# Optimization experiments

Hardware: AMD Instinct MI355X
Metric: run time of the kernel (lower is better)

Reference implementation:

```python
import jax, jax.numpy as jnp
import numpy as np

N = 131072
IN_C1 = 64
MED_C = 64
OUT_C = 64
EPS = 1e-8


def _glorot(key, shape):
    fan_in = shape[0]
    bound = 1.0 / np.sqrt(fan_in)
    return jax.random.uniform(key, shape, jnp.float32, -bound, bound)


def setup_inputs() -> dict:
    key = jax.random.key(0)
    ks = jax.random.split(key, 16)
    inp = {
        "key_value_input": jax.random.normal(ks[0], (N, IN_C1), jnp.float32),
        "query_input": jax.random.normal(ks[1], (N, 7), jnp.float32),
        # Linear params stored as [in, out] (y = x @ W + b)
        "key_W": _glorot(ks[2], (IN_C1, MED_C)), "key_b": jnp.zeros((MED_C,), jnp.float32),
        "value_W": _glorot(ks[3], (IN_C1, MED_C)), "value_b": jnp.zeros((MED_C,), jnp.float32),
        "T_W": _glorot(ks[4], (7, MED_C * MED_C)), "T_b": jnp.zeros((MED_C * MED_C,), jnp.float32),
        "d1_W": _glorot(ks[5], (MED_C, 64)), "d1_b": jnp.zeros((64,), jnp.float32),
        "d2_W": _glorot(ks[6], (64, 32)), "d2_b": jnp.zeros((32,), jnp.float32),
        "d3_W": _glorot(ks[7], (32, OUT_C)), "d3_b": jnp.zeros((OUT_C,), jnp.float32),
        "scale": jnp.float32(1.0),
    }
    return inp


def reference(key_value_input, query_input, key_W, key_b, value_W, value_b,
              T_W, T_b, d1_W, d1_b, d2_W, d2_b, d3_W, d3_b, scale):
    # Per-token hypernetwork: T [N, med_c, med_c]
    T = (query_input @ T_W + T_b).reshape(-1, MED_C, MED_C)
    k = key_value_input @ key_W + key_b              # [N, med_c]
    v = key_value_input @ value_W + value_b          # [N, med_c]
    # query = T @ kv  (batched mat-vec)
    q = jnp.einsum('nij,nj->ni', T, key_value_input)  # [N, med_c]
    att = q * k
    # F.normalize(p=2, dim=-1, eps=1e-8): x / max(||x||_2, eps)
    norm = jnp.linalg.norm(att, axis=-1, keepdims=True)
    att = att / jnp.maximum(norm, EPS)
    v = jax.nn.softmax(v * scale, axis=-1)
    x = att * v
    # small MLP head d
    h = jax.nn.relu(x @ d1_W + d1_b)
    h = jax.nn.relu(h @ d2_W + d2_b)
    return h @ d3_W + d3_b
```

## Files before the change

### kernel.cpp

```cpp
#include <hip/hip_runtime.h>
#include <math.h>

typedef _Float16 f16_t;
typedef __attribute__((ext_vector_type(8))) _Float16 f16x8;
typedef __attribute__((ext_vector_type(4))) float f32x4;

#define NTOK 131072
#define MT   128
#define TPB  256
#define RP16 72
#define OP32 68
#define SLABB 4608

#define OFF_KEY 0
#define OFF_VAL 4096
#define OFF_T   8192
#define OFF_D1  40960
#define OFF_D2  45056
#define OFF_D3  47104
#define WTOT    49152

__device__ __forceinline__ f32x4 mfma1(f16x8 a, f16x8 b, f32x4 c) {
    return __builtin_amdgcn_mfma_f32_16x16x32_f16(a, b, c, 0, 0, 0);
}

struct B2 { f16x8 b0, b1; };

__device__ __forceinline__ B2 loadB_lds(const f16_t* __restrict__ b, int c, int l15, int quad) {
    const char* base = (const char*)b;
    int o0 = (16 * c + l15) * 128 + quad * 16;
    int sw = (l15 & 7) << 4;
    B2 r;
    r.b0 = *(const f16x8*)(base + (o0 ^ sw));
    r.b1 = *(const f16x8*)(base + ((o0 + 64) ^ sw));
    return r;
}

#define GEMML(buf, c, a00, a01, a10, a11, acc0, acc1) do {        \
    B2 Bf = loadB_lds((buf), (c), l15, quad);                      \
    acc0 = mfma1(a01, Bf.b1, mfma1(a00, Bf.b0, acc0));             \
    acc1 = mfma1(a11, Bf.b1, mfma1(a10, Bf.b0, acc1));             \
} while (0)

__device__ __forceinline__ void gl_lds16(const void* g, void* l) {
    __builtin_amdgcn_global_load_lds(
        (const __attribute__((address_space(1))) unsigned int*)g,
        (__attribute__((address_space(3))) unsigned int*)l, 16, 0, 0);
}

__device__ __forceinline__ void stage8k(const f16_t* __restrict__ gsrc, f16_t* lbuf, int tid) {
#pragma unroll
    for (int i = 0; i < 2; ++i) {
        int o = (i * 256 + tid) * 16;
        int g = o ^ (((o >> 7) & 7) << 4);
        gl_lds16((const char*)gsrc + g, (char*)lbuf + (o & ~1023));
    }
}
__device__ __forceinline__ void stage4k_r128(const f16_t* __restrict__ gsrc, f16_t* lbuf, int tid) {
    int o = tid * 16;
    int g = o ^ (((o >> 7) & 7) << 4);
    gl_lds16((const char*)gsrc + g, (char*)lbuf + (o & ~1023));
}
__device__ __forceinline__ void stage4k_r64(const f16_t* __restrict__ gsrc, f16_t* lbuf, int tid) {
    int o = tid * 16;
    int g = o ^ (((o >> 7) & 3) << 4);
    gl_lds16((const char*)gsrc + g, (char*)lbuf + (o & ~1023));
}

#define VMW2() asm volatile("s_waitcnt vmcnt(2)" ::: "memory")
#define VMW0() asm volatile("s_waitcnt vmcnt(0)" ::: "memory")
#define BAR()  do { __builtin_amdgcn_s_barrier(); asm volatile("" ::: "memory"); } while (0)

__global__ __launch_bounds__(256)
void prep_w(const float* __restrict__ keyW, const float* __restrict__ valW,
            const float* __restrict__ TW,   const float* __restrict__ TB,
            const float* __restrict__ d1W,  const float* __restrict__ d2W,
            const float* __restrict__ d3W,  f16_t* __restrict__ wsf)
{
    int idx = blockIdx.x * 256 + threadIdx.x;
    if (idx >= WTOT) return;
    float src;
    if (idx < OFF_VAL) {
        int r = idx - OFF_KEY, n = r >> 6, j = r & 63;
        src = keyW[j * 64 + n];
    } else if (idx < OFF_T) {
        int r = idx - OFF_VAL, n = r >> 6, j = r & 63;
        src = valW[j * 64 + n];
    } else if (idx < OFF_D1) {
        int r = idx - OFF_T, p = r >> 12, q = r & 4095;
        src = (p < 7) ? TW[p * 4096 + q] : TB[q];
    } else if (idx < OFF_D2) {
        int r = idx - OFF_D1, n = r >> 6, j = r & 63;
        src = d1W[j * 64 + n];
    } else if (idx < OFF_D3) {
        int r = idx - OFF_D2, n = r >> 6, j = r & 63;
        src = d2W[j * 32 + n];
    } else {
        int r = idx - OFF_D3, n = r >> 5, j = r & 31;
        src = d3W[j * 64 + n];
    }
    wsf[idx] = (f16_t)src;
}

__device__ __forceinline__ void front_rt(
    f16_t* __restrict__ Rf,
    const f16_t* __restrict__ keyb, const f16_t* __restrict__ valb,
    int l15, int quad, int rtb,
    f16x8 a0, f16x8 a1,
    f32x4 q0, f32x4 q1, f32x4 q2, f32x4 q3,
    f32x4 kbv, f32x4 vbv, float sc)
{
    f32x4 k0 = {}, k1 = {}, k2 = {}, k3 = {}, v0 = {}, v1 = {}, v2 = {}, v3 = {};
    { B2 B = loadB_lds(keyb, 0, l15, quad); k0 = mfma1(a1, B.b1, mfma1(a0, B.b0, k0)); }
    { B2 B = loadB_lds(keyb, 1, l15, quad); k1 = mfma1(a1, B.b1, mfma1(a0, B.b0, k1)); }
    { B2 B = loadB_lds(keyb, 2, l15, quad); k2 = mfma1(a1, B.b1, mfma1(a0, B.b0, k2)); }
    { B2 B = loadB_lds(keyb, 3, l15, quad); k3 = mfma1(a1, B.b1, mfma1(a0, B.b0, k3)); }
    { B2 B = loadB_lds(valb, 0, l15, quad); v0 = mfma1(a1, B.b1, mfma1(a0, B.b0, v0)); }
    { B2 B = loadB_lds(valb, 1, l15, quad); v1 = mfma1(a1, B.b1, mfma1(a0, B.b0, v1)); }
    { B2 B = loadB_lds(valb, 2, l15, quad); v2 = mfma1(a1, B.b1, mfma1(a0, B.b0, v2)); }
    { B2 B = loadB_lds(valb, 3, l15, quad); v3 = mfma1(a1, B.b1, mfma1(a0, B.b0, v3)); }

    f32x4 sv0 = (v0 + vbv[0]) * sc;
    f32x4 sv1 = (v1 + vbv[1]) * sc;
    f32x4 sv2 = (v2 + vbv[2]) * sc;
    f32x4 sv3 = (v3 + vbv[3]) * sc;

    f32x4 mx;
#pragma unroll
    for (int e = 0; e < 4; ++e)
        mx[e] = fmaxf(fmaxf(sv0[e], sv1[e]), fmaxf(sv2[e], sv3[e]));
#pragma unroll
    for (int m = 1; m < 16; m <<= 1)
#pragma unroll
        for (int e = 0; e < 4; ++e) mx[e] = fmaxf(mx[e], __shfl_xor(mx[e], m, 64));
#pragma unroll
    for (int e = 0; e < 4; ++e) {
        sv0[e] = __expf(sv0[e] - mx[e]);
        sv1[e] = __expf(sv1[e] - mx[e]);
        sv2[e] = __expf(sv2[e] - mx[e]);
        sv3[e] = __expf(sv3[e] - mx[e]);
    }
    f32x4 se = sv0 + sv1 + sv2 + sv3;
#pragma unroll
    for (int m = 1; m < 16; m <<= 1)
#pragma unroll
        for (int e = 0; e < 4; ++e) se[e] += __shfl_xor(se[e], m, 64);

    f32x4 at0 = q0 * (k0 + kbv[0]);
    f32x4 at1 = q1 * (k1 + kbv[1]);
    f32x4 at2 = q2 * (k2 + kbv[2]);
    f32x4 at3 = q3 * (k3 + kbv[3]);
    f32x4 nr = at0 * at0 + at1 * at1 + at2 * at2 + at3 * at3;
#pragma unroll
    for (int m = 1; m < 16; m <<= 1)
#pragma unroll
        for (int e = 0; e < 4; ++e) nr[e] += __shfl_xor(nr[e], m, 64);

    f32x4 fac;
#pragma unroll
    for (int e = 0; e < 4; ++e)
        fac[e] = 1.0f / (fmaxf(sqrtf(nr[e]), 1e-8f) * se[e]);

#pragma unroll
    for (int e = 0; e < 4; ++e) {
        f16_t* rr = Rf + (rtb + quad * 4 + e) * RP16 + l15;
        rr[0]  = (f16_t)(at0[e] * sv0[e] * fac[e]);
        rr[16] = (f16_t)(at1[e] * sv1[e] * fac[e]);
        rr[32] = (f16_t)(at2[e] * sv2[e] * fac[e]);
        rr[48] = (f16_t)(at3[e] * sv3[e] * fac[e]);
    }
}

__global__ __launch_bounds__(TPB, 2)
void fused_mfma(const float* __restrict__ kv_in, const float* __restrict__ q_in,
                const float* __restrict__ keyB,  const float* __restrict__ valB,
                const float* __restrict__ d1B,   const float* __restrict__ d2B,
                const float* __restrict__ d3B,   const float* __restrict__ scale_p,
                const f16_t* __restrict__ wsf,   float* __restrict__ out)
{
    __shared__ __align__(16) unsigned char Slab[4][SLABB];
    __shared__ __align__(16) float Qs[8][MT];
    __shared__ __align__(16) f16_t WB[2][4096];

    const int tid  = threadIdx.x;
    const int wv   = tid >> 6, lane = tid & 63;
    const int quad = lane >> 4, l15 = lane & 15;
    const int RB   = wv * 32;
    const long t0  = (long)blockIdx.x * MT;

    f16_t* __restrict__ Rf = (f16_t*)Slab[wv];
    float* __restrict__ Of = (float*)Slab[wv];

    stage8k(wsf + OFF_T + 0 * 4096, WB[0], tid);
    stage8k(wsf + OFF_T + 1 * 4096, WB[1], tid);

    {
        const int r = lane >> 1, half = lane & 1;
        const float4* p4 = (const float4*)(kv_in + (t0 + RB + r) * 64 + half * 32);
        f16_t* dst = Rf + r * RP16 + half * 32;
#pragma unroll
        for (int b = 0; b < 4; ++b) {
            float4 f0 = p4[2 * b], f1 = p4[2 * b + 1];
            f16x8 h;
            h[0] = (f16_t)f0.x; h[1] = (f16_t)f0.y; h[2] = (f16_t)f0.z; h[3] = (f16_t)f0.w;
            h[4] = (f16_t)f1.x; h[5] = (f16_t)f1.y; h[6] = (f16_t)f1.z; h[7] = (f16_t)f1.w;
            *(f16x8*)(dst + 8 * b) = h;
        }
    }
    if (lane < 32) {
        const float* qp = q_in + (t0 + RB + lane) * 7;
#pragma unroll
        for (int p = 0; p < 7; ++p) Qs[p][RB + lane] = qp[p];
        Qs[7][RB + lane] = 1.0f;
    }

    f32x4 kbv, vbv;
#pragma unroll
    for (int c = 0; c < 4; ++c) { kbv[c] = keyB[16 * c + l15]; vbv[c] = valB[16 * c + l15]; }
    const float sc = scale_p[0];

    f16x8 ah00 = *(const f16x8*)(Rf + l15 * RP16 + quad * 8);
    f16x8 ah01 = *(const f16x8*)(Rf + l15 * RP16 + 32 + quad * 8);
    f16x8 ah10 = *(const f16x8*)(Rf + (16 + l15) * RP16 + quad * 8);
    f16x8 ah11 = *(const f16x8*)(Rf + (16 + l15) * RP16 + 32 + quad * 8);

    f32x4 q00 = {}, q01 = {}, q02 = {}, q03 = {};
    f32x4 q10 = {}, q11 = {}, q12 = {}, q13 = {};
#pragma unroll 1
    for (int p = 0; p < 8; ++p) {
        const f16_t* tb = WB[p & 1];
        VMW2(); BAR();
        f32x4 t00 = {}, t01 = {}, t02 = {}, t03 = {};
        f32x4 t10 = {}, t11 = {}, t12 = {}, t13 = {};
        GEMML(tb, 0, ah00, ah01, ah10, ah11, t00, t10);
        GEMML(tb, 1, ah00, ah01, ah10, ah11, t01, t11);
        GEMML(tb, 2, ah00, ah01, ah10, ah11, t02, t12);
        GEMML(tb, 3, ah00, ah01, ah10, ah11, t03, t13);
        f32x4 qp0 = *(const f32x4*)&Qs[p][RB + quad * 4];
        f32x4 qp1 = *(const f32x4*)&Qs[p][RB + 16 + quad * 4];
        q00 += qp0 * t00; q01 += qp0 * t01; q02 += qp0 * t02; q03 += qp0 * t03;
        q10 += qp1 * t10; q11 += qp1 * t11; q12 += qp1 * t12; q13 += qp1 * t13;
        BAR();
        const f16_t* nsrc = (p < 6) ? (wsf + OFF_T + (p + 2) * 4096)
                                    : ((p == 6) ? (wsf + OFF_KEY) : (wsf + OFF_VAL));
        stage8k(nsrc, WB[p & 1], tid);
    }
    VMW0(); BAR();

    front_rt(Rf, WB[0], WB[1], l15, quad, 0,  ah00, ah01, q00, q01, q02, q03, kbv, vbv, sc);
    front_rt(Rf, WB[0], WB[1], l15, quad, 16, ah10, ah11, q10, q11, q12, q13, kbv, vbv, sc);
    BAR();
    stage8k(wsf + OFF_D1, WB[0], tid);
    stage4k_r128(wsf + OFF_D2, WB[1], tid);
    stage4k_r64 (wsf + OFF_D3, WB[1] + 2048, tid);
    VMW0(); BAR();

    f16x8 xh00 = *(const f16x8*)(Rf + l15 * RP16 + quad * 8);
    f16x8 xh01 = *(const f16x8*)(Rf + l15 * RP16 + 32 + quad * 8);
    f16x8 xh10 = *(const f16x8*)(Rf + (16 + l15) * RP16 + quad * 8);
    f16x8 xh11 = *(const f16x8*)(Rf + (16 + l15) * RP16 + 32 + quad * 8);
    {
        f32x4 h00 = {}, h01 = {}, h02 = {}, h03 = {};
        f32x4 h10 = {}, h11 = {}, h12 = {}, h13 = {};
        GEMML(WB[0], 0, xh00, xh01, xh10, xh11, h00, h10);
        GEMML(WB[0], 1, xh00, xh01, xh10, xh11, h01, h11);
        GEMML(WB[0], 2, xh00, xh01, xh10, xh11, h02, h12);
        GEMML(WB[0], 3, xh00, xh01, xh10, xh11, h03, h13);
        f32x4 b1v;
#pragma unroll
        for (int c = 0; c < 4; ++c) b1v[c] = d1B[16 * c + l15];
#pragma unroll
        for (int e = 0; e < 4; ++e) {
            f16_t* r0 = Rf + (quad * 4 + e) * RP16 + l15;
            r0[0]  = (f16_t)fmaxf(h00[e] + b1v[0], 0.f);
            r0[16] = (f16_t)fmaxf(h01[e] + b1v[1], 0.f);
            r0[32] = (f16_t)fmaxf(h02[e] + b1v[2], 0.f);
            r0[48] = (f16_t)fmaxf(h03[e] + b1v[3], 0.f);
            f16_t* r1 = Rf + (16 + quad * 4 + e) * RP16 + l15;
            r1[0]  = (f16_t)fmaxf(h10[e] + b1v[0], 0.f);
            r1[16] = (f16_t)fmaxf(h11[e] + b1v[1], 0.f);
            r1[32] = (f16_t)fmaxf(h12[e] + b1v[2], 0.f);
            r1[48] = (f16_t)fmaxf(h13[e] + b1v[3], 0.f);
        }
    }

    xh00 = *(const f16x8*)(Rf + l15 * RP16 + quad * 8);
    xh01 = *(const f16x8*)(Rf + l15 * RP16 + 32 + quad * 8);
    xh10 = *(const f16x8*)(Rf + (16 + l15) * RP16 + quad * 8);
    xh11 = *(const f16x8*)(Rf + (16 + l15) * RP16 + 32 + quad * 8);
    {
        f32x4 g00 = {}, g01 = {}, g10 = {}, g11 = {};
        GEMML(WB[1], 0, xh00, xh01, xh10, xh11, g00, g10);
        GEMML(WB[1], 1, xh00, xh01, xh10, xh11, g01, g11);
        float b20 = d2B[l15], b21 = d2B[16 + l15];
#pragma unroll
        for (int e = 0; e < 4; ++e) {
            f16_t* r0 = Rf + (quad * 4 + e) * RP16 + l15;
            r0[0]  = (f16_t)fmaxf(g00[e] + b20, 0.f);
            r0[16] = (f16_t)fmaxf(g01[e] + b21, 0.f);
            f16_t* r1 = Rf + (16 + quad * 4 + e) * RP16 + l15;
            r1[0]  = (f16_t)fmaxf(g10[e] + b20, 0.f);
            r1[16] = (f16_t)fmaxf(g11[e] + b21, 0.f);
        }
    }

    f16x8 a30 = *(const f16x8*)(Rf + l15 * RP16 + quad * 8);
    f16x8 a31 = *(const f16x8*)(Rf + (16 + l15) * RP16 + quad * 8);
    f32x4 b3v;
#pragma unroll
    for (int c = 0; c < 4; ++c) b3v[c] = d3B[16 * c + l15];
    float* __restrict__ obase = out + (t0 + RB) * 64;
    const char* d3b = (const char*)(&WB[1][2048]);
    const int sw3 = ((l15 >> 1) & 3) << 4;

#pragma unroll
    for (int h = 0; h < 2; ++h) {
        const f16x8 a3 = h ? a31 : a30;
#pragma unroll
        for (int c = 0; c < 4; ++c) {
            int o3 = (16 * c + l15) * 64 + quad * 16;
            f16x8 bw = *(const f16x8*)(d3b + (o3 ^ sw3));
            f32x4 z = {};
            f32x4 o = mfma1(a3, bw, z);
#pragma unroll
            for (int e = 0; e < 4; ++e)
                Of[(quad * 4 + e) * OP32 + 16 * c + l15] = o[e] + b3v[c];
        }
#pragma unroll
        for (int i = 0; i < 4; ++i) {
            const int r4 = i * 4 + quad;
            f32x4 v = *(const f32x4*)(Of + r4 * OP32 + l15 * 4);
            *(f32x4*)(obase + h * 1024 + i * 256 + lane * 4) = v;
        }
    }
}

extern "C" void kernel_launch(void* const* d_in, const int* in_sizes, int n_in,
                              void* d_out, int out_size, void* d_ws, size_t ws_size,
                              hipStream_t stream) {
    (void)in_sizes; (void)n_in; (void)out_size; (void)ws_size;
    const float* kv_in = (const float*)d_in[0];
    const float* q_in  = (const float*)d_in[1];
    const float* keyW  = (const float*)d_in[2];
    const float* keyB  = (const float*)d_in[3];
    const float* valW  = (const float*)d_in[4];
    const float* valB  = (const float*)d_in[5];
    const float* TW    = (const float*)d_in[6];
    const float* TB    = (const float*)d_in[7];
    const float* d1W   = (const float*)d_in[8];
    const float* d1B   = (const float*)d_in[9];
    const float* d2W   = (const float*)d_in[10];
    const float* d2B   = (const float*)d_in[11];
    const float* d3W   = (const float*)d_in[12];
    const float* d3B   = (const float*)d_in[13];
    const float* scale = (const float*)d_in[14];
    f16_t* wsf = (f16_t*)d_ws;
    float* outp = (float*)d_out;

    prep_w<<<(WTOT + 255) / 256, 256, 0, stream>>>(keyW, valW, TW, TB, d1W, d2W, d3W, wsf);
    fused_mfma<<<NTOK / MT, TPB, 0, stream>>>(kv_in, q_in, keyB, valB,
                                              d1B, d2B, d3B, scale, wsf, outp);
}
```

Before: 135.5 us.

## Double rows per wave to 64 tokens per warp, 256 per block

Raises the token tile from 128 to 256 per block, so each wave handles 64 rows instead of 32. Each T-weight B fragment loaded from LDS now feeds four MFMA row tiles instead of two, and the per-block staging of the hypernetwork and MLP weights is amortized over twice as many tokens. The cost is higher register pressure (16 q accumulators plus 8 A fragments) and twice the LDS slab per wave. The grid halves, which may reduce occupancy and latency hiding.

```diff
diff --git a/kernel.cpp b/kernel.cpp
--- a/kernel.cpp
+++ b/kernel.cpp
@@ -6,11 +6,11 @@
 typedef __attribute__((ext_vector_type(4))) float f32x4;
 
 #define NTOK 131072
-#define MT   128
+#define MT   256
 #define TPB  256
 #define RP16 72
 #define OP32 68
-#define SLABB 4608
+#define SLABB 9216
 
 #define OFF_KEY 0
 #define OFF_VAL 4096
@@ -40,6 +40,19 @@
     B2 Bf = loadB_lds((buf), (c), l15, quad);                      \
     acc0 = mfma1(a01, Bf.b1, mfma1(a00, Bf.b0, acc0));             \
     acc1 = mfma1(a11, Bf.b1, mfma1(a10, Bf.b0, acc1));             \
+} while (0)
+
+#define TCOL(tb, c, QA0, QA1, QA2, QA3, Q0, Q1, Q2, Q3) do {       \
+    B2 Bf = loadB_lds((tb), (c), l15, quad);                        \
+    f32x4 z = {};                                                   \
+    f32x4 tt0 = mfma1(ah01, Bf.b1, mfma1(ah00, Bf.b0, z));          \
+    Q0 += QA0 * tt0;                                                \
+    f32x4 tt1 = mfma1(ah11, Bf.b1, mfma1(ah10, Bf.b0, z));          \
+    Q1 += QA1 * tt1;                                                \
+    f32x4 tt2 = mfma1(ah21, Bf.b1, mfma1(ah20, Bf.b0, z));          \
+    Q2 += QA2 * tt2;                                                \
+    f32x4 tt3 = mfma1(ah31, Bf.b1, mfma1(ah30, Bf.b0, z));          \
+    Q3 += QA3 * tt3;                                                \
 } while (0)
 
 __device__ __forceinline__ void gl_lds16(const void* g, void* l) {
@@ -171,6 +184,85 @@
     }
 }
 
+__device__ __forceinline__ void d1_rt(f16_t* __restrict__ Rf, const f16_t* __restrict__ wb,
+                                      int l15, int quad, int rtb, f32x4 b1v)
+{
+    f16x8 x00 = *(const f16x8*)(Rf + (rtb + l15) * RP16 + quad * 8);
+    f16x8 x01 = *(const f16x8*)(Rf + (rtb + l15) * RP16 + 32 + quad * 8);
+    f16x8 x10 = *(const f16x8*)(Rf + (rtb + 16 + l15) * RP16 + quad * 8);
+    f16x8 x11 = *(const f16x8*)(Rf + (rtb + 16 + l15) * RP16 + 32 + quad * 8);
+    f32x4 h00 = {}, h01 = {}, h02 = {}, h03 = {};
+    f32x4 h10 = {}, h11 = {}, h12 = {}, h13 = {};
+    GEMML(wb, 0, x00, x01, x10, x11, h00, h10);
+    GEMML(wb, 1, x00, x01, x10, x11, h01, h11);
+    GEMML(wb, 2, x00, x01, x10, x11, h02, h12);
+    GEMML(wb, 3, x00, x01, x10, x11, h03, h13);
+#pragma unroll
+    for (int e = 0; e < 4; ++e) {
+        f16_t* r0 = Rf + (rtb + quad * 4 + e) * RP16 + l15;
+        r0[0]  = (f16_t)fmaxf(h00[e] + b1v[0], 0.f);
+        r0[16] = (f16_t)fmaxf(h01[e] + b1v[1], 0.f);
+        r0[32] = (f16_t)fmaxf(h02[e] + b1v[2], 0.f);
+        r0[48] = (f16_t)fmaxf(h03[e] + b1v[3], 0.f);
+        f16_t* r1 = Rf + (rtb + 16 + quad * 4 + e) * RP16 + l15;
+        r1[0]  = (f16_t)fmaxf(h10[e] + b1v[0], 0.f);
+        r1[16] = (f16_t)fmaxf(h11[e] + b1v[1], 0.f);
+        r1[32] = (f16_t)fmaxf(h12[e] + b1v[2], 0.f);
+        r1[48] = (f16_t)fmaxf(h13[e] + b1v[3], 0.f);
+    }
+}
+
+__device__ __forceinline__ void d2_rt(f16_t* __restrict__ Rf, const f16_t* __restrict__ wb,
+                                      int l15, int quad, int rtb, float b20, float b21)
+{
+    f16x8 x00 = *(const f16x8*)(Rf + (rtb + l15) * RP16 + quad * 8);
+    f16x8 x01 = *(const f16x8*)(Rf + (rtb + l15) * RP16 + 32 + quad * 8);
+    f16x8 x10 = *(const f16x8*)(Rf + (rtb + 16 + l15) * RP16 + quad * 8);
+    f16x8 x11 = *(const f16x8*)(Rf + (rtb + 16 + l15) * RP16 + 32 + quad * 8);
+    f32x4 g00 = {}, g01 = {}, g10 = {}, g11 = {};
+    GEMML(wb, 0, x00, x01, x10, x11, g00, g10);
+    GEMML(wb, 1, x00, x01, x10, x11, g01, g11);
+#pragma unroll
+    for (int e = 0; e < 4; ++e) {
+        f16_t* r0 = Rf + (rtb + quad * 4 + e) * RP16 + l15;
+        r0[0]  = (f16_t)fmaxf(g00[e] + b20, 0.f);
+        r0[16] = (f16_t)fmaxf(g01[e] + b21, 0.f);
+        f16_t* r1 = Rf + (rtb + 16 + quad * 4 + e) * RP16 + l15;
+        r1[0]  = (f16_t)fmaxf(g10[e] + b20, 0.f);
+        r1[16] = (f16_t)fmaxf(g11[e] + b21, 0.f);
+    }
+}
+
+__device__ __forceinline__ void d3_rt(f16_t* __restrict__ Rf, float* __restrict__ Of,
+                                      const char* __restrict__ d3b,
+                                      int l15, int quad, int lane, int rtb,
+                                      f32x4 b3v, float* __restrict__ obase)
+{
+    f16x8 a30 = *(const f16x8*)(Rf + (rtb + l15) * RP16 + quad * 8);
+    f16x8 a31 = *(const f16x8*)(Rf + (rtb + 16 + l15) * RP16 + quad * 8);
+    const int sw3 = ((l15 >> 1) & 3) << 4;
+#pragma unroll
+    for (int h = 0; h < 2; ++h) {
+        const f16x8 a3 = h ? a31 : a30;
+#pragma unroll
+        for (int c = 0; c < 4; ++c) {
+            int o3 = (16 * c + l15) * 64 + quad * 16;
+            f16x8 bw = *(const f16x8*)(d3b + (o3 ^ sw3));
+            f32x4 z = {};
+            f32x4 o = mfma1(a3, bw, z);
+#pragma unroll
+            for (int e = 0; e < 4; ++e)
+                Of[(quad * 4 + e) * OP32 + 16 * c + l15] = o[e] + b3v[c];
+        }
+#pragma unroll
+        for (int i = 0; i < 4; ++i) {
+            const int r4 = i * 4 + quad;
+            f32x4 v = *(const f32x4*)(Of + r4 * OP32 + l15 * 4);
+            *(f32x4*)(obase + rtb * 64 + h * 1024 + i * 256 + lane * 4) = v;
+        }
+    }
+}
+
 __global__ __launch_bounds__(TPB, 2)
 void fused_mfma(const float* __restrict__ kv_in, const float* __restrict__ q_in,
                 const float* __restrict__ keyB,  const float* __restrict__ valB,
@@ -185,7 +277,7 @@
     const int tid  = threadIdx.x;
     const int wv   = tid >> 6, lane = tid & 63;
     const int quad = lane >> 4, l15 = lane & 15;
-    const int RB   = wv * 32;
+    const int RB   = wv * 64;
     const long t0  = (long)blockIdx.x * MT;
 
     f16_t* __restrict__ Rf = (f16_t*)Slab[wv];
@@ -194,52 +286,63 @@
     stage8k(wsf + OFF_T + 0 * 4096, WB[0], tid);
     stage8k(wsf + OFF_T + 1 * 4096, WB[1], tid);
 
+    f32x4 kbv, vbv, b1v, b3v;
+#pragma unroll
+    for (int c = 0; c < 4; ++c) {
+        kbv[c] = keyB[16 * c + l15];  vbv[c] = valB[16 * c + l15];
+        b1v[c] = d1B[16 * c + l15];   b3v[c] = d3B[16 * c + l15];
+    }
+    const float b20 = d2B[l15], b21 = d2B[16 + l15];
+    const float sc = scale_p[0];
+
     {
         const int r = lane >> 1, half = lane & 1;
-        const float4* p4 = (const float4*)(kv_in + (t0 + RB + r) * 64 + half * 32);
-        f16_t* dst = Rf + r * RP16 + half * 32;
-#pragma unroll
-        for (int b = 0; b < 4; ++b) {
-            float4 f0 = p4[2 * b], f1 = p4[2 * b + 1];
-            f16x8 h;
-            h[0] = (f16_t)f0.x; h[1] = (f16_t)f0.y; h[2] = (f16_t)f0.z; h[3] = (f16_t)f0.w;
-            h[4] = (f16_t)f1.x; h[5] = (f16_t)f1.y; h[6] = (f16_t)f1.z; h[7] = (f16_t)f1.w;
-            *(f16x8*)(dst + 8 * b) = h;
+#pragma unroll
+        for (int s = 0; s < 2; ++s) {
+            const float4* p4 = (const float4*)(kv_in + (t0 + RB + s * 32 + r) * 64 + half * 32);
+            f16_t* dst = Rf + (s * 32 + r) * RP16 + half * 32;
+#pragma unroll
+            for (int b = 0; b < 4; ++b) {
+                float4 f0 = p4[2 * b], f1 = p4[2 * b + 1];
+                f16x8 h;
+                h[0] = (f16_t)f0.x; h[1] = (f16_t)f0.y; h[2] = (f16_t)f0.z; h[3] = (f16_t)f0.w;
+                h[4] = (f16_t)f1.x; h[5] = (f16_t)f1.y; h[6] = (f16_t)f1.z; h[7] = (f16_t)f1.w;
+                *(f16x8*)(dst + 8 * b) = h;
+            }
         }
     }
-    if (lane < 32) {
+    {
         const float* qp = q_in + (t0 + RB + lane) * 7;
 #pragma unroll
         for (int p = 0; p < 7; ++p) Qs[p][RB + lane] = qp[p];
         Qs[7][RB + lane] = 1.0f;
     }
-
-    f32x4 kbv, vbv;
-#pragma unroll
-    for (int c = 0; c < 4; ++c) { kbv[c] = keyB[16 * c + l15]; vbv[c] = valB[16 * c + l15]; }
-    const float sc = scale_p[0];
 
     f16x8 ah00 = *(const f16x8*)(Rf + l15 * RP16 + quad * 8);
     f16x8 ah01 = *(const f16x8*)(Rf + l15 * RP16 + 32 + quad * 8);
     f16x8 ah10 = *(const f16x8*)(Rf + (16 + l15) * RP16 + quad * 8);
     f16x8 ah11 = *(const f16x8*)(Rf + (16 + l15) * RP16 + 32 + quad * 8);
+    f16x8 ah20 = *(const f16x8*)(Rf + (32 + l15) * RP16 + quad * 8);
+    f16x8 ah21 = *(const f16x8*)(Rf + (32 + l15) * RP16 + 32 + quad * 8);
+    f16x8 ah30 = *(const f16x8*)(Rf + (48 + l15) * RP16 + quad * 8);
+    f16x8 ah31 = *(const f16x8*)(Rf + (48 + l15) * RP16 + 32 + quad * 8);
 
     f32x4 q00 = {}, q01 = {}, q02 = {}, q03 = {};
     f32x4 q10 = {}, q11 = {}, q12 = {}, q13 = {};
+    f32x4 q20 = {}, q21 = {}, q22 = {}, q23 = {};
+    f32x4 q30 = {}, q31 = {}, q32 = {}, q33 = {};
 #pragma unroll 1
     for (int p = 0; p < 8; ++p) {
         const f16_t* tb = WB[p & 1];
         VMW2(); BAR();
-        f32x4 t00 = {}, t01 = {}, t02 = {}, t03 = {};
-        f32x4 t10 = {}, t11 = {}, t12 = {}, t13 = {};
-        GEMML(tb, 0, ah00, ah01, ah10, ah11, t00, t10);
-        GEMML(tb, 1, ah00, ah01, ah10, ah11, t01, t11);
-        GEMML(tb, 2, ah00, ah01, ah10, ah11, t02, t12);
-        GEMML(tb, 3, ah00, ah01, ah10, ah11, t03, t13);
-        f32x4 qp0 = *(const f32x4*)&Qs[p][RB + quad * 4];
-        f32x4 qp1 = *(const f32x4*)&Qs[p][RB + 16 + quad * 4];
-        q00 += qp0 * t00; q01 += qp0 * t01; q02 += qp0 * t02; q03 += qp0 * t03;
-        q10 += qp1 * t10; q11 += qp1 * t11; q12 += qp1 * t12; q13 += qp1 * t13;
+        f32x4 qa0 = *(const f32x4*)&Qs[p][RB + quad * 4];
+        f32x4 qa1 = *(const f32x4*)&Qs[p][RB + 16 + quad * 4];
+        f32x4 qa2 = *(const f32x4*)&Qs[p][RB + 32 + quad * 4];
+        f32x4 qa3 = *(const f32x4*)&Qs[p][RB + 48 + quad * 4];
+        TCOL(tb, 0, qa0, qa1, qa2, qa3, q00, q10, q20, q30);
+        TCOL(tb, 1, qa0, qa1, qa2, qa3, q01, q11, q21, q31);
+        TCOL(tb, 2, qa0, qa1, qa2, qa3, q02, q12, q22, q32);
+        TCOL(tb, 3, qa0, qa1, qa2, qa3, q03, q13, q23, q33);
         BAR();
         const f16_t* nsrc = (p < 6) ? (wsf + OFF_T + (p + 2) * 4096)
                                     : ((p == 6) ? (wsf + OFF_KEY) : (wsf + OFF_VAL));
@@ -249,90 +352,23 @@
 
     front_rt(Rf, WB[0], WB[1], l15, quad, 0,  ah00, ah01, q00, q01, q02, q03, kbv, vbv, sc);
     front_rt(Rf, WB[0], WB[1], l15, quad, 16, ah10, ah11, q10, q11, q12, q13, kbv, vbv, sc);
+    front_rt(Rf, WB[0], WB[1], l15, quad, 32, ah20, ah21, q20, q21, q22, q23, kbv, vbv, sc);
+    front_rt(Rf, WB[0], WB[1], l15, quad, 48, ah30, ah31, q30, q31, q32, q33, kbv, vbv, sc);
     BAR();
     stage8k(wsf + OFF_D1, WB[0], tid);
     stage4k_r128(wsf + OFF_D2, WB[1], tid);
     stage4k_r64 (wsf + OFF_D3, WB[1] + 2048, tid);
     VMW0(); BAR();
 
-    f16x8 xh00 = *(const f16x8*)(Rf + l15 * RP16 + quad * 8);
-    f16x8 xh01 = *(const f16x8*)(Rf + l15 * RP16 + 32 + quad * 8);
-    f16x8 xh10 = *(const f16x8*)(Rf + (16 + l15) * RP16 + quad * 8);
-    f16x8 xh11 = *(const f16x8*)(Rf + (16 + l15) * RP16 + 32 + quad * 8);
-    {
-        f32x4 h00 = {}, h01 = {}, h02 = {}, h03 = {};
-        f32x4 h10 = {}, h11 = {}, h12 = {}, h13 = {};
-        GEMML(WB[0], 0, xh00, xh01, xh10, xh11, h00, h10);
-        GEMML(WB[0], 1, xh00, xh01, xh10, xh11, h01, h11);
-        GEMML(WB[0], 2, xh00, xh01, xh10, xh11, h02, h12);
-        GEMML(WB[0], 3, xh00, xh01, xh10, xh11, h03, h13);
-        f32x4 b1v;
-#pragma unroll
-        for (int c = 0; c < 4; ++c) b1v[c] = d1B[16 * c + l15];
-#pragma unroll
-        for (int e = 0; e < 4; ++e) {
-            f16_t* r0 = Rf + (quad * 4 + e) * RP16 + l15;
-            r0[0]  = (f16_t)fmaxf(h00[e] + b1v[0], 0.f);
-            r0[16] = (f16_t)fmaxf(h01[e] + b1v[1], 0.f);
-            r0[32] = (f16_t)fmaxf(h02[e] + b1v[2], 0.f);
-            r0[48] = (f16_t)fmaxf(h03[e] + b1v[3], 0.f);
-            f16_t* r1 = Rf + (16 + quad * 4 + e) * RP16 + l15;
-            r1[0]  = (f16_t)fmaxf(h10[e] + b1v[0], 0.f);
-            r1[16] = (f16_t)fmaxf(h11[e] + b1v[1], 0.f);
-            r1[32] = (f16_t)fmaxf(h12[e] + b1v[2], 0.f);
-            r1[48] = (f16_t)fmaxf(h13[e] + b1v[3], 0.f);
-        }
-    }
-
-    xh00 = *(const f16x8*)(Rf + l15 * RP16 + quad * 8);
-    xh01 = *(const f16x8*)(Rf + l15 * RP16 + 32 + quad * 8);
-    xh10 = *(const f16x8*)(Rf + (16 + l15) * RP16 + quad * 8);
-    xh11 = *(const f16x8*)(Rf + (16 + l15) * RP16 + 32 + quad * 8);
-    {
-        f32x4 g00 = {}, g01 = {}, g10 = {}, g11 = {};
-        GEMML(WB[1], 0, xh00, xh01, xh10, xh11, g00, g10);
-        GEMML(WB[1], 1, xh00, xh01, xh10, xh11, g01, g11);
-        float b20 = d2B[l15], b21 = d2B[16 + l15];
-#pragma unroll
-        for (int e = 0; e < 4; ++e) {
-            f16_t* r0 = Rf + (quad * 4 + e) * RP16 + l15;
-            r0[0]  = (f16_t)fmaxf(g00[e] + b20, 0.f);
-            r0[16] = (f16_t)fmaxf(g01[e] + b21, 0.f);
-            f16_t* r1 = Rf + (16 + quad * 4 + e) * RP16 + l15;
-            r1[0]  = (f16_t)fmaxf(g10[e] + b20, 0.f);
-            r1[16] = (f16_t)fmaxf(g11[e] + b21, 0.f);
-        }
-    }
-
-    f16x8 a30 = *(const f16x8*)(Rf + l15 * RP16 + quad * 8);
-    f16x8 a31 = *(const f16x8*)(Rf + (16 + l15) * RP16 + quad * 8);
-    f32x4 b3v;
-#pragma unroll
-    for (int c = 0; c < 4; ++c) b3v[c] = d3B[16 * c + l15];
+    d1_rt(Rf, WB[0], l15, quad, 0,  b1v);
+    d1_rt(Rf, WB[0], l15, quad, 32, b1v);
+    d2_rt(Rf, WB[1], l15, quad, 0,  b20, b21);
+    d2_rt(Rf, WB[1], l15, quad, 32, b20, b21);
+
     float* __restrict__ obase = out + (t0 + RB) * 64;
     const char* d3b = (const char*)(&WB[1][2048]);
-    const int sw3 = ((l15 >> 1) & 3) << 4;
-
-#pragma unroll
-    for (int h = 0; h < 2; ++h) {
-        const f16x8 a3 = h ? a31 : a30;
-#pragma unroll
-        for (int c = 0; c < 4; ++c) {
-            int o3 = (16 * c + l15) * 64 + quad * 16;
-            f16x8 bw = *(const f16x8*)(d3b + (o3 ^ sw3));
-            f32x4 z = {};
-            f32x4 o = mfma1(a3, bw, z);
-#pragma unroll
-            for (int e = 0; e < 4; ++e)
-                Of[(quad * 4 + e) * OP32 + 16 * c + l15] = o[e] + b3v[c];
-        }
-#pragma unroll
-        for (int i = 0; i < 4; ++i) {
-            const int r4 = i * 4 + quad;
-            f32x4 v = *(const f32x4*)(Of + r4 * OP32 + l15 * 4);
-            *(f32x4*)(obase + h * 1024 + i * 256 + lane * 4) = v;
-        }
-    }
+    d3_rt(Rf, Of, d3b, l15, quad, lane, 0,  b3v, obase);
+    d3_rt(Rf, Of, d3b, l15, quad, lane, 32, b3v, obase);
 }
 
 extern "C" void kernel_launch(void* const* d_in, const int* in_sizes, int n_in,
```

New measurement: 130.0 us. 1.04x faster.
